# Optimization experiments

Measured on AMD Instinct MI355X. Metric: run time of the kernel, lower is better.

The kernel has to match this reference:

```python
import jax, jax.numpy as jnp
import numpy as np

B, D, H = 4096, 66, 512  # batch, system dim (22 atoms * 3), MLP hidden


def _dynamics(t, xs, W1, b1, W2, b2, W3, b3):
    # CNF vector field f(t, x): 3-layer SiLU MLP on concat([x, t])
    h = jnp.concatenate([xs, t], axis=1)          # [B, D+1]
    h = jax.nn.silu(h @ W1 + b1)                  # [B, H]
    h = jax.nn.silu(h @ W2 + b2)                  # [B, H]
    return h @ W3 + b3                            # [B, D]


def setup_inputs() -> dict:
    key = jax.random.key(0)
    ks = jax.random.split(key, 5)
    xs = jax.random.normal(ks[0], (B, D), dtype=jnp.float32)
    t = jax.random.uniform(ks[1], (B, 1), dtype=jnp.float32)
    W1 = jax.random.normal(ks[2], (D + 1, H), dtype=jnp.float32) / np.float32(np.sqrt(D + 1))
    b1 = jnp.zeros((H,), dtype=jnp.float32)
    W2 = jax.random.normal(ks[3], (H, H), dtype=jnp.float32) / np.float32(np.sqrt(H))
    b2 = jnp.zeros((H,), dtype=jnp.float32)
    W3 = jax.random.normal(ks[4], (H, D), dtype=jnp.float32) / np.float32(np.sqrt(H))
    b3 = jnp.zeros((D,), dtype=jnp.float32)
    return {"xs": xs, "t": t, "W1": W1, "b1": b1, "W2": W2, "b2": b2, "W3": W3, "b3": b3}


def reference(xs, t, W1, b1, W2, b2, W3, b3):
    # Exact divergence: trace of Jacobian d f / d x, computed with D JVPs
    # (forward-mode equivalent of the torch per-dim autograd.grad loop).
    def f(x):
        return _dynamics(t, x, W1, b1, W2, b2, W3, b3)

    dxs = f(xs)                                   # [B, D]
    eye = jnp.eye(D, dtype=xs.dtype)              # basis vectors e_i

    def jvp_col(e):
        _, tang = jax.jvp(f, (xs,), (jnp.broadcast_to(e, xs.shape),))
        return tang                               # J @ e_i, shape [B, D]

    tangs = jax.vmap(jvp_col)(eye)                # [D, B, D]
    div = jnp.einsum('dbd->b', tangs)             # sum_i (J e_i)_i = tr(J)
    return dxs, -div[:, None]
```

## Files before the change

### kernel.cpp

```cpp
#include <hip/hip_runtime.h>

#define Bn 4096
#define Dn 66
#define Hn 512

typedef __attribute__((ext_vector_type(8))) short short8;
typedef __attribute__((ext_vector_type(4))) float f32x4;

__device__ __forceinline__ unsigned short f2bf(float x) {
    union { float f; unsigned u; } v; v.f = x;
    unsigned r = v.u + 0x7fffu + ((v.u >> 16) & 1u);
    return (unsigned short)(r >> 16);
}
__device__ __forceinline__ float bf2f(unsigned short h) {
    union { float f; unsigned u; } v; v.u = ((unsigned)h) << 16; return v.f;
}


__global__ __launch_bounds__(512, 2) void k_prep(
    const float* __restrict__ xs, const float* __restrict__ tt,
    const float* __restrict__ W1, const float* __restrict__ b1,
    const float* __restrict__ W2, const float* __restrict__ W3,
    unsigned short* __restrict__ W2P, unsigned short* __restrict__ CmP,
    unsigned short* __restrict__ W3P,
    unsigned short* __restrict__ h1hiP, unsigned short* __restrict__ h1loP,
    unsigned short* __restrict__ s1P)
{
    __shared__ float sX[67*16];
    const int bid = blockIdx.x, tid = threadIdx.x;
    const int lane = tid & 63, wv = tid >> 6;

    if (bid < 256) {
        const int rt = bid, r0 = rt*16;
        for (int idx = tid; idx < 67*16; idx += 512) {
            const int i = idx >> 4, r = idx & 15;
            sX[idx] = (i < Dn) ? xs[(size_t)(r0+r)*Dn + i] : tt[r0+r];
        }
        __syncthreads();
        const int rg = lane & 7, cg = lane >> 3;
        const int cA = wv*64 + cg*4, cB = cA + 32;
        float z[2][8];
        {
            const float4 bA4 = *(const float4*)&b1[cA];
            const float4 bB4 = *(const float4*)&b1[cB];
            const float bb[8] = {bA4.x,bA4.y,bA4.z,bA4.w, bB4.x,bB4.y,bB4.z,bB4.w};
            #pragma unroll
            for (int j = 0; j < 8; ++j) { z[0][j] = bb[j]; z[1][j] = bb[j]; }
        }
        for (int i = 0; i < 67; ++i) {
            const float2 xf = *(const float2*)&sX[i*16 + 2*rg];
            const float4 wA = *(const float4*)&W1[(size_t)i*Hn + cA];
            const float4 wB = *(const float4*)&W1[(size_t)i*Hn + cB];
            const float ww[8] = {wA.x,wA.y,wA.z,wA.w, wB.x,wB.y,wB.z,wB.w};
            #pragma unroll
            for (int j = 0; j < 8; ++j) {
                z[0][j] = fmaf(xf.x, ww[j], z[0][j]);
                z[1][j] = fmaf(xf.y, ww[j], z[1][j]);
            }
        }
        const int kgrp = cg >> 1, joff = (cg & 1)*4;
        #pragma unroll
        for (int rr = 0; rr < 2; ++rr) {
            const int r = 2*rg + rr;
            #pragma unroll
            for (int grp = 0; grp < 2; ++grp) {
                ushort4 phi, plo, ps;
                unsigned short* PH = (unsigned short*)&phi;
                unsigned short* PL = (unsigned short*)&plo;
                unsigned short* PS = (unsigned short*)&ps;
                #pragma unroll
                for (int j = 0; j < 4; ++j) {
                    const float zv = z[rr][grp*4 + j];
                    const float sg = 1.f / (1.f + __expf(-zv));
                    const float h  = zv * sg;
                    const float sp = sg * (1.f + zv * (1.f - sg));
                    const unsigned short hh = f2bf(h);
                    PH[j] = hh;
                    PL[j] = f2bf(h - bf2f(hh));
                    PS[j] = f2bf(sp);
                }
                const int ks = 2*wv + grp;
                const size_t off = ((size_t)(rt*16 + ks)*64 + r + 16*kgrp)*8 + joff;
                *(ushort4*)&h1hiP[off] = phi;
                *(ushort4*)&h1loP[off] = plo;
                *(ushort4*)&s1P [off] = ps;
            }
        }
    } else if (bid < 320) {
        const int tix = (bid - 256)*8 + wv;
        const int ks = tix & 15;
        const int n = lane & 15, kg = lane >> 4;
        const int c = (tix >> 4)*16 + n;
        const int abase = ks*32 + kg*8;
        float w2v[8], m[8];
        #pragma unroll
        for (int j = 0; j < 8; ++j) {
            w2v[j] = W2[(size_t)(abase + j)*Hn + c];
            m[j] = 0.f;
        }
        for (int i = 0; i < Dn; ++i) {
            const float w3 = W3[(size_t)c*Dn + i];
            const float4 w1a = *(const float4*)&W1[(size_t)i*Hn + abase];
            const float4 w1b = *(const float4*)&W1[(size_t)i*Hn + abase + 4];
            m[0] = fmaf(w3, w1a.x, m[0]); m[1] = fmaf(w3, w1a.y, m[1]);
            m[2] = fmaf(w3, w1a.z, m[2]); m[3] = fmaf(w3, w1a.w, m[3]);
            m[4] = fmaf(w3, w1b.x, m[4]); m[5] = fmaf(w3, w1b.y, m[5]);
            m[6] = fmaf(w3, w1b.z, m[6]); m[7] = fmaf(w3, w1b.w, m[7]);
        }
        short8 pw, pc;
        #pragma unroll
        for (int j = 0; j < 8; ++j) {
            pw[j] = (short)f2bf(w2v[j]);
            pc[j] = (short)f2bf(w2v[j] * m[j]);
        }
        const size_t off = ((size_t)tix*64 + lane)*8;
        *(short8*)&W2P[off] = pw;
        *(short8*)&CmP[off] = pc;
    } else {
        const int tix = (bid - 320)*8 + wv;
        if (tix < 80) {
            const int ks = tix & 15;
            const int n = lane & 15, kg = lane >> 4;
            const int j_out = (tix >> 4)*16 + n;
            const int abase = ks*32 + kg*8;
            short8 p;
            #pragma unroll
            for (int j = 0; j < 8; ++j)
                p[j] = (j_out < Dn) ? (short)f2bf(W3[(size_t)(abase + j)*Dn + j_out]) : (short)0;
            *(short8*)&W3P[((size_t)tix*64 + lane)*8] = p;
        }
    }
}

__global__ __launch_bounds__(512, 2) void k_fuse23(
    const unsigned short* __restrict__ h1hiP, const unsigned short* __restrict__ h1loP,
    const unsigned short* __restrict__ s1P,
    const unsigned short* __restrict__ W2P, const unsigned short* __restrict__ CmP,
    const float* __restrict__ b2,
    const unsigned short* __restrict__ W3P, const float* __restrict__ b3,
    float* __restrict__ out)
{
    __shared__ __align__(16) unsigned short sH[16*Hn];
    __shared__ __align__(16) unsigned short sL[16*Hn];
    __shared__ float sRed[8*16];
    const int tid = threadIdx.x, lane = tid & 63, wv = tid >> 6;
    const int rt = blockIdx.x;
    const int r0 = rt*16;
    const int ctb = wv*4;
    const int n = lane & 15, kg = lane >> 4;

    f32x4 zac[4], vac[4];
    #pragma unroll
    for (int ti = 0; ti < 4; ++ti) {
        const float bz = b2[(ctb + ti)*16 + n];
        zac[ti] = (f32x4){bz, bz, bz, bz};
        vac[ti] = (f32x4){0.f, 0.f, 0.f, 0.f};
    }
    #pragma unroll 2
    for (int ks = 0; ks < 16; ++ks) {
        const size_t aoff = ((size_t)(rt*16 + ks)*64 + lane)*8;
        const short8 ahi = *(const short8*)&h1hiP[aoff];
        const short8 alo = *(const short8*)&h1loP[aoff];
        const short8 as1 = *(const short8*)&s1P [aoff];
        #pragma unroll
        for (int ti = 0; ti < 4; ++ti) {
            const size_t wo = ((size_t)((ctb + ti)*16 + ks)*64 + lane)*8;
            const short8 wf = *(const short8*)&W2P[wo];
            const short8 qf = *(const short8*)&CmP[wo];
            zac[ti] = __builtin_amdgcn_mfma_f32_16x16x32_bf16(ahi, wf, zac[ti], 0, 0, 0);
            zac[ti] = __builtin_amdgcn_mfma_f32_16x16x32_bf16(alo, wf, zac[ti], 0, 0, 0);
            vac[ti] = __builtin_amdgcn_mfma_f32_16x16x32_bf16(as1, qf, vac[ti], 0, 0, 0);
        }
    }

    float dp[4] = {0.f, 0.f, 0.f, 0.f};
    #pragma unroll
    for (int ti = 0; ti < 4; ++ti) {
        const int c = (ctb + ti)*16 + n;
        const int ks2 = c >> 5, kg2 = (c >> 3) & 3, j2 = c & 7;
        #pragma unroll
        for (int q = 0; q < 4; ++q) {
            const float z2 = zac[ti][q];
            const float sg = 1.f / (1.f + __expf(-z2));
            const float h2 = z2 * sg;
            dp[q] = fmaf(sg * (1.f + z2 * (1.f - sg)), vac[ti][q], dp[q]);
            const unsigned short hh = f2bf(h2);
            const int o = (ks2*64 + (kg*4 + q) + 16*kg2)*8 + j2;
            sH[o] = hh;
            sL[o] = f2bf(h2 - bf2f(hh));
        }
    }
    #pragma unroll
    for (int q = 0; q < 4; ++q) {
        float v = dp[q];
        v += __shfl_xor(v, 1, 64);
        v += __shfl_xor(v, 2, 64);
        v += __shfl_xor(v, 4, 64);
        v += __shfl_xor(v, 8, 64);
        if (n == 0) sRed[wv*16 + kg*4 + q] = v;
    }
    __syncthreads();

    if (tid < 16) {
        float s = 0.f;
        #pragma unroll
        for (int q = 0; q < 8; ++q) s += sRed[q*16 + tid];
        out[(size_t)Bn*Dn + r0 + tid] = -s;
    }

    if (wv < 5) {
        const int jt = wv;
        const int j = jt*16 + n;
        const float bj = (j < Dn) ? b3[j] : 0.f;
        f32x4 oac = (f32x4){bj, bj, bj, bj};
        #pragma unroll 4
        for (int ks = 0; ks < 16; ++ks) {
            const int aoff = (ks*64 + lane)*8;
            const short8 ahi = *(const short8*)&sH[aoff];
            const short8 alo = *(const short8*)&sL[aoff];
            const short8 wf  = *(const short8*)&W3P[((size_t)(jt*16 + ks)*64 + lane)*8];
            oac = __builtin_amdgcn_mfma_f32_16x16x32_bf16(ahi, wf, oac, 0, 0, 0);
            oac = __builtin_amdgcn_mfma_f32_16x16x32_bf16(alo, wf, oac, 0, 0, 0);
        }
        if (j < Dn) {
            #pragma unroll
            for (int q = 0; q < 4; ++q)
                out[(size_t)(r0 + kg*4 + q)*Dn + j] = oac[q];
        }
    }
}

extern "C" void kernel_launch(void* const* d_in, const int* in_sizes, int n_in,
                              void* d_out, int out_size, void* d_ws, size_t ws_size,
                              hipStream_t stream)
{
    const float* xs = (const float*)d_in[0];
    const float* t  = (const float*)d_in[1];
    const float* W1 = (const float*)d_in[2];
    const float* b1 = (const float*)d_in[3];
    const float* W2 = (const float*)d_in[4];
    const float* b2 = (const float*)d_in[5];
    const float* W3 = (const float*)d_in[6];
    const float* b3 = (const float*)d_in[7];
    float* out = (float*)d_out;

    char* ws = (char*)d_ws;
    unsigned short* W2P  = (unsigned short*)(ws);
    unsigned short* CmP  = (unsigned short*)(ws + 524288);
    unsigned short* W3P  = (unsigned short*)(ws + 1048576);
    unsigned short* h1hi = (unsigned short*)(ws + 1130496);
    unsigned short* h1lo = (unsigned short*)(ws + 5324800);
    unsigned short* s1   = (unsigned short*)(ws + 9519104);

    k_prep  <<<330, 512, 0, stream>>>(xs, t, W1, b1, W2, W3, W2P, CmP, W3P, h1hi, h1lo, s1);
    k_fuse23<<<256, 512, 0, stream>>>(h1hi, h1lo, s1, W2P, CmP, b2, W3P, b3, out);
}
```

Baseline: 118.5 us.

## Fuse layer-1 compute into main kernel via LDS, split weight packing out

The layer-1 activations (hi/lo bf16 split and SiLU derivative) are now computed per 16-row tile inside the main kernel and kept in shared memory, not written to and reread from global workspace. Weight packing moves into its own small kernel that runs first. This removes about 12 MB of global round-trip traffic. The cost is more LDS per block (about 48 KB extra), which may reduce occupancy, and the layer-1 FMA work now sits on the main kernel's critical path instead of overlapping with weight packing.

```diff
diff --git a/kernel.cpp b/kernel.cpp
--- a/kernel.cpp
+++ b/kernel.cpp
@@ -17,26 +17,86 @@
 }
 
 
-__global__ __launch_bounds__(512, 2) void k_prep(
+__global__ __launch_bounds__(512, 2) void k_pack(
+    const float* __restrict__ W1, const float* __restrict__ W2,
+    const float* __restrict__ W3,
+    unsigned short* __restrict__ W2P, unsigned short* __restrict__ CmP,
+    unsigned short* __restrict__ W3P)
+{
+    const int bid = blockIdx.x, tid = threadIdx.x;
+    const int lane = tid & 63, wv = tid >> 6;
+
+    if (bid < 64) {
+        const int tix = bid*8 + wv;
+        const int ks = tix & 15;
+        const int n = lane & 15, kg = lane >> 4;
+        const int c = (tix >> 4)*16 + n;
+        const int abase = ks*32 + kg*8;
+        float w2v[8], m[8];
+        #pragma unroll
+        for (int j = 0; j < 8; ++j) {
+            w2v[j] = W2[(size_t)(abase + j)*Hn + c];
+            m[j] = 0.f;
+        }
+        for (int i = 0; i < Dn; ++i) {
+            const float w3 = W3[(size_t)c*Dn + i];
+            const float4 w1a = *(const float4*)&W1[(size_t)i*Hn + abase];
+            const float4 w1b = *(const float4*)&W1[(size_t)i*Hn + abase + 4];
+            m[0] = fmaf(w3, w1a.x, m[0]); m[1] = fmaf(w3, w1a.y, m[1]);
+            m[2] = fmaf(w3, w1a.z, m[2]); m[3] = fmaf(w3, w1a.w, m[3]);
+            m[4] = fmaf(w3, w1b.x, m[4]); m[5] = fmaf(w3, w1b.y, m[5]);
+            m[6] = fmaf(w3, w1b.z, m[6]); m[7] = fmaf(w3, w1b.w, m[7]);
+        }
+        short8 pw, pc;
+        #pragma unroll
+        for (int j = 0; j < 8; ++j) {
+            pw[j] = (short)f2bf(w2v[j]);
+            pc[j] = (short)f2bf(w2v[j] * m[j]);
+        }
+        const size_t off = ((size_t)tix*64 + lane)*8;
+        *(short8*)&W2P[off] = pw;
+        *(short8*)&CmP[off] = pc;
+    } else {
+        const int tix = (bid - 64)*8 + wv;
+        if (tix < 80) {
+            const int ks = tix & 15;
+            const int n = lane & 15, kg = lane >> 4;
+            const int j_out = (tix >> 4)*16 + n;
+            const int abase = ks*32 + kg*8;
+            short8 p;
+            #pragma unroll
+            for (int j = 0; j < 8; ++j)
+                p[j] = (j_out < Dn) ? (short)f2bf(W3[(size_t)(abase + j)*Dn + j_out]) : (short)0;
+            *(short8*)&W3P[((size_t)tix*64 + lane)*8] = p;
+        }
+    }
+}
+
+__global__ __launch_bounds__(512, 2) void k_main(
     const float* __restrict__ xs, const float* __restrict__ tt,
     const float* __restrict__ W1, const float* __restrict__ b1,
-    const float* __restrict__ W2, const float* __restrict__ W3,
-    unsigned short* __restrict__ W2P, unsigned short* __restrict__ CmP,
-    unsigned short* __restrict__ W3P,
-    unsigned short* __restrict__ h1hiP, unsigned short* __restrict__ h1loP,
-    unsigned short* __restrict__ s1P)
+    const unsigned short* __restrict__ W2P, const unsigned short* __restrict__ CmP,
+    const float* __restrict__ b2,
+    const unsigned short* __restrict__ W3P, const float* __restrict__ b3,
+    float* __restrict__ out)
 {
+    __shared__ __align__(16) unsigned short sA[3*8192];
+    __shared__ __align__(16) unsigned short sH[8192];
+    __shared__ __align__(16) unsigned short sL[8192];
     __shared__ float sX[67*16];
-    const int bid = blockIdx.x, tid = threadIdx.x;
-    const int lane = tid & 63, wv = tid >> 6;
-
-    if (bid < 256) {
-        const int rt = bid, r0 = rt*16;
-        for (int idx = tid; idx < 67*16; idx += 512) {
-            const int i = idx >> 4, r = idx & 15;
-            sX[idx] = (i < Dn) ? xs[(size_t)(r0+r)*Dn + i] : tt[r0+r];
-        }
-        __syncthreads();
+    __shared__ float sRed[8*16];
+
+    const int tid = threadIdx.x, lane = tid & 63, wv = tid >> 6;
+    const int rt = blockIdx.x, r0 = rt*16;
+    const int n = lane & 15, kg = lane >> 4;
+
+    for (int idx = tid; idx < 67*16; idx += 512) {
+        const int i = idx >> 4, r = idx & 15;
+        sX[idx] = (i < Dn) ? xs[(size_t)(r0+r)*Dn + i] : tt[r0+r];
+    }
+    __syncthreads();
+
+    {
         const int rg = lane & 7, cg = lane >> 3;
         const int cA = wv*64 + cg*4, cB = cA + 32;
         float z[2][8];
@@ -80,75 +140,16 @@
                     PS[j] = f2bf(sp);
                 }
                 const int ks = 2*wv + grp;
-                const size_t off = ((size_t)(rt*16 + ks)*64 + r + 16*kgrp)*8 + joff;
-                *(ushort4*)&h1hiP[off] = phi;
-                *(ushort4*)&h1loP[off] = plo;
-                *(ushort4*)&s1P [off] = ps;
+                const int off = (ks*64 + r + 16*kgrp)*8 + joff;
+                *(ushort4*)&sA[off]          = phi;
+                *(ushort4*)&sA[8192 + off]   = plo;
+                *(ushort4*)&sA[16384 + off]  = ps;
             }
         }
-    } else if (bid < 320) {
-        const int tix = (bid - 256)*8 + wv;
-        const int ks = tix & 15;
-        const int n = lane & 15, kg = lane >> 4;
-        const int c = (tix >> 4)*16 + n;
-        const int abase = ks*32 + kg*8;
-        float w2v[8], m[8];
-        #pragma unroll
-        for (int j = 0; j < 8; ++j) {
-            w2v[j] = W2[(size_t)(abase + j)*Hn + c];
-            m[j] = 0.f;
-        }
-        for (int i = 0; i < Dn; ++i) {
-            const float w3 = W3[(size_t)c*Dn + i];
-            const float4 w1a = *(const float4*)&W1[(size_t)i*Hn + abase];
-            const float4 w1b = *(const float4*)&W1[(size_t)i*Hn + abase + 4];
-            m[0] = fmaf(w3, w1a.x, m[0]); m[1] = fmaf(w3, w1a.y, m[1]);
-            m[2] = fmaf(w3, w1a.z, m[2]); m[3] = fmaf(w3, w1a.w, m[3]);
-            m[4] = fmaf(w3, w1b.x, m[4]); m[5] = fmaf(w3, w1b.y, m[5]);
-            m[6] = fmaf(w3, w1b.z, m[6]); m[7] = fmaf(w3, w1b.w, m[7]);
-        }
-        short8 pw, pc;
-        #pragma unroll
-        for (int j = 0; j < 8; ++j) {
-            pw[j] = (short)f2bf(w2v[j]);
-            pc[j] = (short)f2bf(w2v[j] * m[j]);
-        }
-        const size_t off = ((size_t)tix*64 + lane)*8;
-        *(short8*)&W2P[off] = pw;
-        *(short8*)&CmP[off] = pc;
-    } else {
-        const int tix = (bid - 320)*8 + wv;
-        if (tix < 80) {
-            const int ks = tix & 15;
-            const int n = lane & 15, kg = lane >> 4;
-            const int j_out = (tix >> 4)*16 + n;
-            const int abase = ks*32 + kg*8;
-            short8 p;
-            #pragma unroll
-            for (int j = 0; j < 8; ++j)
-                p[j] = (j_out < Dn) ? (short)f2bf(W3[(size_t)(abase + j)*Dn + j_out]) : (short)0;
-            *(short8*)&W3P[((size_t)tix*64 + lane)*8] = p;
-        }
-    }
-}
-
-__global__ __launch_bounds__(512, 2) void k_fuse23(
-    const unsigned short* __restrict__ h1hiP, const unsigned short* __restrict__ h1loP,
-    const unsigned short* __restrict__ s1P,
-    const unsigned short* __restrict__ W2P, const unsigned short* __restrict__ CmP,
-    const float* __restrict__ b2,
-    const unsigned short* __restrict__ W3P, const float* __restrict__ b3,
-    float* __restrict__ out)
-{
-    __shared__ __align__(16) unsigned short sH[16*Hn];
-    __shared__ __align__(16) unsigned short sL[16*Hn];
-    __shared__ float sRed[8*16];
-    const int tid = threadIdx.x, lane = tid & 63, wv = tid >> 6;
-    const int rt = blockIdx.x;
-    const int r0 = rt*16;
+    }
+    __syncthreads();
+
     const int ctb = wv*4;
-    const int n = lane & 15, kg = lane >> 4;
-
     f32x4 zac[4], vac[4];
     #pragma unroll
     for (int ti = 0; ti < 4; ++ti) {
@@ -158,10 +159,10 @@
     }
     #pragma unroll 2
     for (int ks = 0; ks < 16; ++ks) {
-        const size_t aoff = ((size_t)(rt*16 + ks)*64 + lane)*8;
-        const short8 ahi = *(const short8*)&h1hiP[aoff];
-        const short8 alo = *(const short8*)&h1loP[aoff];
-        const short8 as1 = *(const short8*)&s1P [aoff];
+        const int ao = (ks*64 + lane)*8;
+        const short8 ahi = *(const short8*)&sA[ao];
+        const short8 alo = *(const short8*)&sA[8192 + ao];
+        const short8 as1 = *(const short8*)&sA[16384 + ao];
         #pragma unroll
         for (int ti = 0; ti < 4; ++ti) {
             const size_t wo = ((size_t)((ctb + ti)*16 + ks)*64 + lane)*8;
@@ -245,13 +246,10 @@
     float* out = (float*)d_out;
 
     char* ws = (char*)d_ws;
-    unsigned short* W2P  = (unsigned short*)(ws);
-    unsigned short* CmP  = (unsigned short*)(ws + 524288);
-    unsigned short* W3P  = (unsigned short*)(ws + 1048576);
-    unsigned short* h1hi = (unsigned short*)(ws + 1130496);
-    unsigned short* h1lo = (unsigned short*)(ws + 5324800);
-    unsigned short* s1   = (unsigned short*)(ws + 9519104);
-
-    k_prep  <<<330, 512, 0, stream>>>(xs, t, W1, b1, W2, W3, W2P, CmP, W3P, h1hi, h1lo, s1);
-    k_fuse23<<<256, 512, 0, stream>>>(h1hi, h1lo, s1, W2P, CmP, b2, W3P, b3, out);
-}
+    unsigned short* W2P = (unsigned short*)(ws);
+    unsigned short* CmP = (unsigned short*)(ws + 524288);
+    unsigned short* W3P = (unsigned short*)(ws + 1048576);
+
+    k_pack<<<74,  512, 0, stream>>>(W1, W2, W3, W2P, CmP, W3P);
+    k_main<<<256, 512, 0, stream>>>(xs, t, W1, b1, W2P, CmP, b2, W3P, b3, out);
+}
```

After: 118.5 us. No clear change (+0.0%).
